# Kernel tuning notes

Measured on AMD Instinct MI355X. Metric: run time of the kernel, lower is better.

The kernel has to match this reference:

```python
import jax, jax.numpy as jnp
import numpy as np

N = 100000
E = 1600000
IN_DIM = 128
HID = 128
OUT_DIM = 128


def _glorot(key, shape):
    lim = jnp.sqrt(6.0 / (shape[0] + shape[1]))
    return jax.random.uniform(key, shape, jnp.float32, -lim, lim)


def setup_inputs() -> dict:
    key = jax.random.key(0)
    ks = jax.random.split(key, 8)
    x = jax.random.normal(ks[0], (N, IN_DIM), jnp.float32)
    edge_index = jax.random.randint(ks[1], (2, E), 0, N, jnp.int64)
    # layer 1 (SAGEConv(in_dim, hid)): lin_l applied to mean-aggregated neighbors (with bias),
    # lin_r applied to root features (no bias) -- PyG SAGEConv semantics.
    W1l = _glorot(ks[2], (IN_DIM, HID))
    b1l = jnp.zeros((HID,), jnp.float32)
    W1r = _glorot(ks[3], (IN_DIM, HID))
    # layer 2 (SAGEConv(hid, out_dim))
    W2l = _glorot(ks[4], (HID, OUT_DIM))
    b2l = jnp.zeros((OUT_DIM,), jnp.float32)
    W2r = _glorot(ks[5], (HID, OUT_DIM))
    return {"x": x, "edge_index": edge_index,
            "W1l": W1l, "b1l": b1l, "W1r": W1r,
            "W2l": W2l, "b2l": b2l, "W2r": W2r}


def _sage_conv(h, src, dst, Wl, bl, Wr):
    # mean aggregation of source features onto target nodes
    msg_sum = jax.ops.segment_sum(h[src], dst, num_segments=N)  # [N, d]
    deg = jax.ops.segment_sum(jnp.ones((src.shape[0],), h.dtype), dst, num_segments=N)
    agg = msg_sum / jnp.maximum(deg, 1.0)[:, None]
    return agg @ Wl + bl + h @ Wr


def reference(x, edge_index, W1l, b1l, W1r, W2l, b2l, W2r):
    src = edge_index[0]
    dst = edge_index[1]
    h = jax.nn.relu(_sage_conv(x, src, dst, W1l, b1l, W1r))
    h = _sage_conv(h, src, dst, W2l, b2l, W2r)
    return h
```

## Files before the change

### kernel.cpp

```cpp
#include <hip/hip_runtime.h>
#include <cstdint>
#include <cstddef>

#define NN 100000
#define EE 1600000
#define DIM 128
#define CAP 48
#define OVF_CAP 512

#define NB 391
#define BCAP 4608
#define SLOTS 32
#define FLUSH_AT 16
#define ACHUNK 4096

typedef __attribute__((ext_vector_type(8))) short bf16x8;
typedef __attribute__((ext_vector_type(4))) float f32x4;

__device__ __forceinline__ unsigned short f2bf(float f) {
  union { float f; uint32_t u; } v; v.f = f;
  uint32_t r = v.u + 0x7FFF + ((v.u >> 16) & 1);
  return (unsigned short)(r >> 16);
}
__device__ __forceinline__ float bf2f(unsigned short s) {
  union { uint32_t u; float f; } v; v.u = (uint32_t)s << 16;
  return v.f;
}
__device__ __forceinline__ float uaf(uint32_t u) {
  union { uint32_t u; float f; } v; v.u = u;
  return v.f;
}

__global__ __launch_bounds__(256) void partA_kernel(
    const void* __restrict__ edges, int* __restrict__ bcnt,
    unsigned* __restrict__ part, int* __restrict__ novf, int* __restrict__ ovf) {
  __shared__ unsigned stage[NB][SLOTS + 1];
  __shared__ int scnt[NB];
  __shared__ int sh_i64;
  const int t = threadIdx.x;
  for (int b = t; b < NB; b += 256) scnt[b] = 0;
  if (t < 64) {
    int v = ((const int*)edges)[2 * t + 1];
    unsigned long long m = __ballot(v != 0);
    if (t == 0) sh_i64 = (m == 0ull) ? 1 : 0;
  }
  __syncthreads();
  const int i64 = sh_i64;
  const long long ebase = (long long)blockIdx.x * ACHUNK;
  const int nrounds = ACHUNK / 256;
  for (int r = 0; r < nrounds; ++r) {
    long long e = ebase + (long long)r * 256 + t;
    if (e < EE) {
      int s, d;
      if (i64) {
        s = (int)((const long long*)edges)[e];
        d = (int)((const long long*)edges)[(long long)EE + e];
      } else {
        s = ((const int*)edges)[e];
        d = ((const int*)edges)[(long long)EE + e];
      }
      if ((unsigned)s < NN && (unsigned)d < NN) {
        int b = d >> 8;
        unsigned pk = (unsigned)s | ((unsigned)(d & 255) << 17);
        int pos = atomicAdd(&scnt[b], 1);
        if (pos < SLOTS) {
          stage[b][pos] = pk;
        } else {
          int g = atomicAdd(&bcnt[b], 1);
          if (g < BCAP) part[(size_t)b * BCAP + g] = pk;
          else { int oi = atomicAdd(novf, 1); if (oi < OVF_CAP) { ovf[oi*2] = s; ovf[oi*2+1] = d; } }
        }
      }
    }
    __syncthreads();
    const bool last = (r == nrounds - 1);
    for (int b = t; b < NB; b += 256) {
      int c = scnt[b];
      if (c > SLOTS) c = SLOTS;
      if (c > 0 && (last || c >= FLUSH_AT)) {
        int g = atomicAdd(&bcnt[b], c);
        for (int i = 0; i < c; ++i) {
          int gp = g + i;
          unsigned pk = stage[b][i];
          if (gp < BCAP) {
            part[(size_t)b * BCAP + gp] = pk;
          } else {
            int oi = atomicAdd(novf, 1);
            if (oi < OVF_CAP) { ovf[oi*2] = (int)(pk & 0x1FFFF); ovf[oi*2+1] = (b << 8) | (int)(pk >> 17); }
          }
        }
        scnt[b] = 0;
      }
    }
    __syncthreads();
  }
}

__global__ __launch_bounds__(256) void partB_kernel(
    const int* __restrict__ bcnt, const unsigned* __restrict__ part,
    int* __restrict__ cnt, int* __restrict__ ell,
    int* __restrict__ novf, int* __restrict__ ovf) {
  __shared__ int lcnt[256];
  __shared__ int lell[256 * CAP];
  const int t = threadIdx.x;
  const int b = blockIdx.x;
  lcnt[t] = 0;
  __syncthreads();
  int n = bcnt[b];
  if (n > BCAP) n = BCAP;
  for (int i = t; i < n; i += 256) {
    unsigned pk = part[(size_t)b * BCAP + i];
    int s = (int)(pk & 0x1FFFF);
    int dl = (int)(pk >> 17);
    int pos = atomicAdd(&lcnt[dl], 1);
    if (pos < CAP) lell[dl * CAP + pos] = s;
    else { int oi = atomicAdd(novf, 1); if (oi < OVF_CAP) { ovf[oi*2] = s; ovf[oi*2+1] = (b << 8) | dl; } }
  }
  __syncthreads();
  int4* dst = (int4*)(ell + (size_t)b * 256 * CAP);
  const int4* src = (const int4*)lell;
#pragma unroll
  for (int i = 0; i < 256 * CAP / 4 / 256; ++i) dst[t + i * 256] = src[t + i * 256];
  int node = b * 256 + t;
  if (node < NN) cnt[node] = lcnt[t];
}

__global__ void prep_kernel(const float* __restrict__ x,
                            const float* __restrict__ W1l, const float* __restrict__ W1r,
                            const float* __restrict__ W2l, const float* __restrict__ W2r,
                            unsigned short* __restrict__ Wt1, unsigned short* __restrict__ Wt2,
                            unsigned short* __restrict__ xhi) {
  if (blockIdx.x < 256) {
    int idx = blockIdx.x * 256 + threadIdx.x;
    int layer = idx >> 15;
    int rest = idx & 32767;
    int mat = rest >> 14;
    int r = rest & 16383;
    int k = r >> 7, n = r & 127;
    const float* W = layer ? (mat ? W2r : W2l) : (mat ? W1r : W1l);
    unsigned short* Wt = layer ? Wt2 : Wt1;
    Wt[((size_t)(mat * 128 + n)) * 128 + k] = f2bf(W[k * 128 + n]);
  } else {
    int i = (blockIdx.x - 256) * 256 + threadIdx.x;
    if (i >= NN * DIM / 4) return;
    f32x4 v = ((const f32x4*)x)[i];
    ushort4 hi;
    hi.x = f2bf(v[0]); hi.y = f2bf(v[1]); hi.z = f2bf(v[2]); hi.w = f2bf(v[3]);
    ((ushort4*)xhi)[i] = hi;
  }
}

__device__ __forceinline__ void acc_dw4(float* s, uint4 w) {
  s[0] += uaf(w.x << 16); s[1] += uaf(w.x & 0xFFFF0000u);
  s[2] += uaf(w.y << 16); s[3] += uaf(w.y & 0xFFFF0000u);
  s[4] += uaf(w.z << 16); s[5] += uaf(w.z & 0xFFFF0000u);
  s[6] += uaf(w.w << 16); s[7] += uaf(w.w & 0xFFFF0000u);
}

__global__ __launch_bounds__(256) void gather_ell_kernel(
    const int* __restrict__ cnt, const int* __restrict__ ell,
    const unsigned short* __restrict__ h, unsigned short* __restrict__ ahi,
    const int* __restrict__ novf, const int* __restrict__ ovf) {
  const int node = blockIdx.x * 4 + (threadIdx.x >> 6);
  const int lane = threadIdx.x & 63;
  const int q = lane >> 4;
  const int l = lane & 15;
  if (node >= NN) return;
  const int dcnt = cnt[node];
  const int n = dcnt < CAP ? dcnt : CAP;
  const int* row = ell + (size_t)node * CAP;
  float s[8] = {0.f, 0.f, 0.f, 0.f, 0.f, 0.f, 0.f, 0.f};
  int p = q;
  for (; p + 12 < n; p += 16) {
    uint4 w0 = *(const uint4*)(h + (size_t)row[p] * DIM + l * 8);
    uint4 w1 = *(const uint4*)(h + (size_t)row[p + 4] * DIM + l * 8);
    uint4 w2 = *(const uint4*)(h + (size_t)row[p + 8] * DIM + l * 8);
    uint4 w3 = *(const uint4*)(h + (size_t)row[p + 12] * DIM + l * 8);
    acc_dw4(s, w0);
    acc_dw4(s, w1);
    acc_dw4(s, w2);
    acc_dw4(s, w3);
  }
  for (; p < n; p += 4) {
    uint4 w0 = *(const uint4*)(h + (size_t)row[p] * DIM + l * 8);
    acc_dw4(s, w0);
  }
#pragma unroll
  for (int i = 0; i < 8; ++i) {
    s[i] += __shfl_xor(s[i], 16, 64);
    s[i] += __shfl_xor(s[i], 32, 64);
  }
  if (q == 0) {
    if (dcnt > CAP) {
      int no = *novf;
      if (no > OVF_CAP) no = OVF_CAP;
      for (int i = 0; i < no; ++i) {
        if (ovf[i * 2 + 1] == node) {
          uint4 w0 = *(const uint4*)(h + (size_t)ovf[i * 2] * DIM + l * 8);
          acc_dw4(s, w0);
        }
      }
    }
    const float rd = 1.0f / fmaxf((float)dcnt, 1.0f);
    ushort4 o0, o1;
    o0.x = f2bf(s[0] * rd); o0.y = f2bf(s[1] * rd);
    o0.z = f2bf(s[2] * rd); o0.w = f2bf(s[3] * rd);
    o1.x = f2bf(s[4] * rd); o1.y = f2bf(s[5] * rd);
    o1.z = f2bf(s[6] * rd); o1.w = f2bf(s[7] * rd);
    *(ushort4*)(ahi + (size_t)node * DIM + l * 8) = o0;
    *(ushort4*)(ahi + (size_t)node * DIM + l * 8 + 4) = o1;
  }
}

template <bool RELU, bool WPLANES, bool WOUT>
__global__ __launch_bounds__(256, 2) void dense_mfma_kernel(
    const unsigned short* __restrict__ ahi, const unsigned short* __restrict__ hhi,
    const unsigned short* __restrict__ Wt, const float* __restrict__ bl,
    float* __restrict__ out, unsigned short* __restrict__ phi, int n) {
  const int t = threadIdx.x;
  const int wave = t >> 6, lane = t & 63;
  const int l15 = lane & 15, l4 = lane >> 4;
  const int base = blockIdx.x * 64;

  bf16x8 bfr[2][4][2];
#pragma unroll
  for (int mat = 0; mat < 2; ++mat)
#pragma unroll
    for (int kt = 0; kt < 4; ++kt)
#pragma unroll
      for (int ntl = 0; ntl < 2; ++ntl) {
        int ncol = (wave * 2 + ntl) * 16 + l15;
        int k0 = kt * 32 + l4 * 8;
        bfr[mat][kt][ntl] = *(const bf16x8*)(Wt + ((size_t)(mat * 128 + ncol)) * 128 + k0);
      }

  f32x4 acc[4][2];
#pragma unroll
  for (int ntl = 0; ntl < 2; ++ntl) {
    float b = bl[(wave * 2 + ntl) * 16 + l15];
#pragma unroll
    for (int rt = 0; rt < 4; ++rt) {
      f32x4 ib = {b, b, b, b};
      acc[rt][ntl] = ib;
    }
  }

#pragma unroll
  for (int kt = 0; kt < 4; ++kt) {
    const int k0 = kt * 32 + l4 * 8;
#pragma unroll
    for (int rt = 0; rt < 4; ++rt) {
      int row = base + rt * 16 + l15;
      if (row >= n) row = n - 1;
      const size_t off = (size_t)row * DIM + k0;
      bf16x8 a8 = *(const bf16x8*)(ahi + off);
      bf16x8 hh8 = *(const bf16x8*)(hhi + off);
#pragma unroll
      for (int ntl = 0; ntl < 2; ++ntl) {
        acc[rt][ntl] = __builtin_amdgcn_mfma_f32_16x16x32_bf16(a8, bfr[0][kt][ntl], acc[rt][ntl], 0, 0, 0);
        acc[rt][ntl] = __builtin_amdgcn_mfma_f32_16x16x32_bf16(hh8, bfr[1][kt][ntl], acc[rt][ntl], 0, 0, 0);
      }
    }
  }

  __syncthreads();

#pragma unroll
  for (int rt = 0; rt < 4; ++rt)
#pragma unroll
    for (int ntl = 0; ntl < 2; ++ntl) {
      const int col = (wave * 2 + ntl) * 16 + l15;
#pragma unroll
      for (int r = 0; r < 4; ++r) {
        int row = base + rt * 16 + l4 * 4 + r;
        if (row < n) {
          float v = acc[rt][ntl][r];
          if (RELU) v = fmaxf(v, 0.f);
          const size_t off = (size_t)row * DIM + col;
          if (WOUT) out[off] = v;
          if (WPLANES) phi[off] = f2bf(v);
        }
      }
    }
}

extern "C" void kernel_launch(void* const* d_in, const int* in_sizes, int n_in,
                              void* d_out, int out_size, void* d_ws, size_t ws_size,
                              hipStream_t stream) {
  const float* x   = (const float*)d_in[0];
  const void* edges = d_in[1];
  const float* W1l = (const float*)d_in[2];
  const float* b1l = (const float*)d_in[3];
  const float* W1r = (const float*)d_in[4];
  const float* W2l = (const float*)d_in[5];
  const float* b2l = (const float*)d_in[6];
  const float* W2r = (const float*)d_in[7];
  float* out = (float*)d_out;

  char* p = (char*)d_ws;
  unsigned short* Wt1 = (unsigned short*)p;               p += 2 * 128 * 128 * 2;
  unsigned short* Wt2 = (unsigned short*)p;               p += 2 * 128 * 128 * 2;
  int* cnt  = (int*)p;                                    p += (size_t)NN * 4;
  int* bcnt = (int*)p;                                    p += (size_t)NB * 4;
  int* novf = (int*)p;                                    p += 4;
  p = (char*)(((uintptr_t)p + 15) & ~(uintptr_t)15);
  int* ovf = (int*)p;                                     p += (size_t)OVF_CAP * 2 * 4;
  p = (char*)(((uintptr_t)p + 255) & ~(uintptr_t)255);
  int* ell = (int*)p;                                     p += (size_t)NB * 256 * CAP * 4;
  p = (char*)(((uintptr_t)p + 255) & ~(uintptr_t)255);
  unsigned short* hhi = (unsigned short*)p;               p += (size_t)NN * DIM * 2;
  unsigned short* ahi = (unsigned short*)p;               p += (size_t)NN * DIM * 2;
  unsigned* part = (unsigned*)ahi;

  hipMemsetAsync(bcnt, 0, ((size_t)NB + 1) * 4, stream);

  partA_kernel<<<(EE + ACHUNK - 1) / ACHUNK, 256, 0, stream>>>(edges, bcnt, part, novf, ovf);
  partB_kernel<<<NB, 256, 0, stream>>>(bcnt, part, cnt, ell, novf, ovf);

  prep_kernel<<<256 + NN * DIM / 4 / 256, 256, 0, stream>>>(x, W1l, W1r, W2l, W2r, Wt1, Wt2, hhi);

  const int gather_blocks = (NN + 3) / 4;
  const int dense_blocks = (NN + 63) / 64;

  gather_ell_kernel<<<gather_blocks, 256, 0, stream>>>(cnt, ell, hhi, ahi, novf, ovf);
  dense_mfma_kernel<true, true, false><<<dense_blocks, 256, 0, stream>>>(
      ahi, hhi, Wt1, b1l, out, hhi, NN);

  gather_ell_kernel<<<gather_blocks, 256, 0, stream>>>(cnt, ell, hhi, ahi, novf, ovf);
  dense_mfma_kernel<false, false, true><<<dense_blocks, 256, 0, stream>>>(
      ahi, hhi, Wt2, b2l, out, nullptr, NN);
}
```

Measured before the change: 270.3 us.

## Fuse neighbor gather with MFMA dense layer and merge prep into partition kernel

The gather and the dense MFMA kernels are merged into one per-layer kernel. Each block aggregates 64 nodes (two nodes per wave iteration) into a swizzled LDS tile, then runs the bf16 MFMA GEMM reading A from LDS, which removes the global round-trip of the aggregated matrix. The weight/x bf16 prep work is folded into the edge partition kernel as extra blocks, and that kernel now runs 512 threads per block, which saves a launch. Layer-2 reads go to a separate hh1 buffer so they no longer alias hx. Risks are lower gather parallelism per block, load imbalance across nodes with different degrees, and weights being reloaded per k-tile instead of being held in registers.

```diff
diff --git a/kernel.cpp b/kernel.cpp
--- a/kernel.cpp
+++ b/kernel.cpp
@@ -13,6 +13,10 @@
 #define SLOTS 32
 #define FLUSH_AT 16
 #define ACHUNK 4096
+#define ATHREADS 512
+
+#define NPREP_W 128
+#define NPREP_X ((NN * DIM / 4) / ATHREADS)
 
 typedef __attribute__((ext_vector_type(8))) short bf16x8;
 typedef __attribute__((ext_vector_type(4))) float f32x4;
@@ -22,23 +26,58 @@
   uint32_t r = v.u + 0x7FFF + ((v.u >> 16) & 1);
   return (unsigned short)(r >> 16);
 }
-__device__ __forceinline__ float bf2f(unsigned short s) {
-  union { uint32_t u; float f; } v; v.u = (uint32_t)s << 16;
-  return v.f;
-}
 __device__ __forceinline__ float uaf(uint32_t u) {
   union { uint32_t u; float f; } v; v.u = u;
   return v.f;
 }
-
-__global__ __launch_bounds__(256) void partA_kernel(
+__device__ __forceinline__ uint32_t pk2(float a, float b) {
+  return (uint32_t)f2bf(a) | ((uint32_t)f2bf(b) << 16);
+}
+__device__ __forceinline__ void acc_dw4(float* s, uint4 w) {
+  s[0] += uaf(w.x << 16); s[1] += uaf(w.x & 0xFFFF0000u);
+  s[2] += uaf(w.y << 16); s[3] += uaf(w.y & 0xFFFF0000u);
+  s[4] += uaf(w.z << 16); s[5] += uaf(w.z & 0xFFFF0000u);
+  s[6] += uaf(w.w << 16); s[7] += uaf(w.w & 0xFFFF0000u);
+}
+
+__global__ __launch_bounds__(ATHREADS) void partA_prep_kernel(
     const void* __restrict__ edges, int* __restrict__ bcnt,
-    unsigned* __restrict__ part, int* __restrict__ novf, int* __restrict__ ovf) {
+    unsigned* __restrict__ part, int* __restrict__ novf, int* __restrict__ ovf,
+    const float* __restrict__ x,
+    const float* __restrict__ W1l, const float* __restrict__ W1r,
+    const float* __restrict__ W2l, const float* __restrict__ W2r,
+    unsigned short* __restrict__ Wt1, unsigned short* __restrict__ Wt2,
+    unsigned short* __restrict__ xhi) {
   __shared__ unsigned stage[NB][SLOTS + 1];
   __shared__ int scnt[NB];
   __shared__ int sh_i64;
   const int t = threadIdx.x;
-  for (int b = t; b < NB; b += 256) scnt[b] = 0;
+
+  if (blockIdx.x >= NB) {
+    int bid = blockIdx.x - NB;
+    if (bid < NPREP_W) {
+      int idx = bid * ATHREADS + t;
+      int layer = idx >> 15;
+      int rest = idx & 32767;
+      int mat = rest >> 14;
+      int r = rest & 16383;
+      int k = r >> 7, n = r & 127;
+      const float* W = layer ? (mat ? W2r : W2l) : (mat ? W1r : W1l);
+      unsigned short* Wt = layer ? Wt2 : Wt1;
+      Wt[((size_t)(mat * 128 + n)) * 128 + k] = f2bf(W[k * 128 + n]);
+    } else {
+      int i = (bid - NPREP_W) * ATHREADS + t;
+      if (i < NN * DIM / 4) {
+        f32x4 v = ((const f32x4*)x)[i];
+        ushort4 hi;
+        hi.x = f2bf(v[0]); hi.y = f2bf(v[1]); hi.z = f2bf(v[2]); hi.w = f2bf(v[3]);
+        ((ushort4*)xhi)[i] = hi;
+      }
+    }
+    return;
+  }
+
+  for (int b = t; b < NB; b += ATHREADS) scnt[b] = 0;
   if (t < 64) {
     int v = ((const int*)edges)[2 * t + 1];
     unsigned long long m = __ballot(v != 0);
@@ -47,9 +86,9 @@
   __syncthreads();
   const int i64 = sh_i64;
   const long long ebase = (long long)blockIdx.x * ACHUNK;
-  const int nrounds = ACHUNK / 256;
+  const int nrounds = ACHUNK / ATHREADS;
   for (int r = 0; r < nrounds; ++r) {
-    long long e = ebase + (long long)r * 256 + t;
+    long long e = ebase + (long long)r * ATHREADS + t;
     if (e < EE) {
       int s, d;
       if (i64) {
@@ -74,7 +113,7 @@
     }
     __syncthreads();
     const bool last = (r == nrounds - 1);
-    for (int b = t; b < NB; b += 256) {
+    for (int b = t; b < NB; b += ATHREADS) {
       int c = scnt[b];
       if (c > SLOTS) c = SLOTS;
       if (c > 0 && (last || c >= FLUSH_AT)) {
@@ -125,115 +164,85 @@
   if (node < NN) cnt[node] = lcnt[t];
 }
 
-__global__ void prep_kernel(const float* __restrict__ x,
-                            const float* __restrict__ W1l, const float* __restrict__ W1r,
-                            const float* __restrict__ W2l, const float* __restrict__ W2r,
-                            unsigned short* __restrict__ Wt1, unsigned short* __restrict__ Wt2,
-                            unsigned short* __restrict__ xhi) {
-  if (blockIdx.x < 256) {
-    int idx = blockIdx.x * 256 + threadIdx.x;
-    int layer = idx >> 15;
-    int rest = idx & 32767;
-    int mat = rest >> 14;
-    int r = rest & 16383;
-    int k = r >> 7, n = r & 127;
-    const float* W = layer ? (mat ? W2r : W2l) : (mat ? W1r : W1l);
-    unsigned short* Wt = layer ? Wt2 : Wt1;
-    Wt[((size_t)(mat * 128 + n)) * 128 + k] = f2bf(W[k * 128 + n]);
-  } else {
-    int i = (blockIdx.x - 256) * 256 + threadIdx.x;
-    if (i >= NN * DIM / 4) return;
-    f32x4 v = ((const f32x4*)x)[i];
-    ushort4 hi;
-    hi.x = f2bf(v[0]); hi.y = f2bf(v[1]); hi.z = f2bf(v[2]); hi.w = f2bf(v[3]);
-    ((ushort4*)xhi)[i] = hi;
-  }
-}
-
-__device__ __forceinline__ void acc_dw4(float* s, uint4 w) {
-  s[0] += uaf(w.x << 16); s[1] += uaf(w.x & 0xFFFF0000u);
-  s[2] += uaf(w.y << 16); s[3] += uaf(w.y & 0xFFFF0000u);
-  s[4] += uaf(w.z << 16); s[5] += uaf(w.z & 0xFFFF0000u);
-  s[6] += uaf(w.w << 16); s[7] += uaf(w.w & 0xFFFF0000u);
-}
-
-__global__ __launch_bounds__(256) void gather_ell_kernel(
+template <bool RELU, bool WPLANES, bool WOUT>
+__global__ __launch_bounds__(256, 3) void fused_kernel(
     const int* __restrict__ cnt, const int* __restrict__ ell,
-    const unsigned short* __restrict__ h, unsigned short* __restrict__ ahi,
+    const unsigned short* __restrict__ h, const unsigned short* __restrict__ Wt,
+    const float* __restrict__ bl, float* __restrict__ out,
+    unsigned short* __restrict__ ph,
     const int* __restrict__ novf, const int* __restrict__ ovf) {
-  const int node = blockIdx.x * 4 + (threadIdx.x >> 6);
-  const int lane = threadIdx.x & 63;
+  __shared__ unsigned short lds_a[64 * DIM];
+  const int t = threadIdx.x;
+  const int wave = t >> 6, lane = t & 63;
   const int q = lane >> 4;
   const int l = lane & 15;
-  if (node >= NN) return;
-  const int dcnt = cnt[node];
-  const int n = dcnt < CAP ? dcnt : CAP;
-  const int* row = ell + (size_t)node * CAP;
-  float s[8] = {0.f, 0.f, 0.f, 0.f, 0.f, 0.f, 0.f, 0.f};
-  int p = q;
-  for (; p + 12 < n; p += 16) {
-    uint4 w0 = *(const uint4*)(h + (size_t)row[p] * DIM + l * 8);
-    uint4 w1 = *(const uint4*)(h + (size_t)row[p + 4] * DIM + l * 8);
-    uint4 w2 = *(const uint4*)(h + (size_t)row[p + 8] * DIM + l * 8);
-    uint4 w3 = *(const uint4*)(h + (size_t)row[p + 12] * DIM + l * 8);
-    acc_dw4(s, w0);
-    acc_dw4(s, w1);
-    acc_dw4(s, w2);
-    acc_dw4(s, w3);
-  }
-  for (; p < n; p += 4) {
-    uint4 w0 = *(const uint4*)(h + (size_t)row[p] * DIM + l * 8);
-    acc_dw4(s, w0);
-  }
-#pragma unroll
-  for (int i = 0; i < 8; ++i) {
-    s[i] += __shfl_xor(s[i], 16, 64);
-    s[i] += __shfl_xor(s[i], 32, 64);
-  }
-  if (q == 0) {
-    if (dcnt > CAP) {
-      int no = *novf;
-      if (no > OVF_CAP) no = OVF_CAP;
-      for (int i = 0; i < no; ++i) {
-        if (ovf[i * 2 + 1] == node) {
-          uint4 w0 = *(const uint4*)(h + (size_t)ovf[i * 2] * DIM + l * 8);
-          acc_dw4(s, w0);
+  const int base = blockIdx.x * 64;
+
+  for (int i = 0; i < 16; i += 2) {
+    const int nl0 = wave * 16 + i;
+    const int nl1 = nl0 + 1;
+    const int node0 = base + nl0, node1 = base + nl1;
+    const int dc0 = (node0 < NN) ? cnt[node0] : 0;
+    const int dc1 = (node1 < NN) ? cnt[node1] : 0;
+    const int n0 = dc0 < CAP ? dc0 : CAP;
+    const int n1 = dc1 < CAP ? dc1 : CAP;
+    const int* r0 = ell + (size_t)node0 * CAP;
+    const int* r1 = ell + (size_t)node1 * CAP;
+    float s0[8] = {0.f,0.f,0.f,0.f,0.f,0.f,0.f,0.f};
+    float s1[8] = {0.f,0.f,0.f,0.f,0.f,0.f,0.f,0.f};
+    const int nmax = n0 > n1 ? n0 : n1;
+    for (int p = q; p < nmax; p += 16) {
+      uint4 w[8];
+#pragma unroll
+      for (int j = 0; j < 4; ++j)
+        if (p + j * 4 < n0) w[j] = *(const uint4*)(h + (size_t)r0[p + j * 4] * DIM + l * 8);
+#pragma unroll
+      for (int j = 0; j < 4; ++j)
+        if (p + j * 4 < n1) w[4 + j] = *(const uint4*)(h + (size_t)r1[p + j * 4] * DIM + l * 8);
+#pragma unroll
+      for (int j = 0; j < 4; ++j)
+        if (p + j * 4 < n0) acc_dw4(s0, w[j]);
+#pragma unroll
+      for (int j = 0; j < 4; ++j)
+        if (p + j * 4 < n1) acc_dw4(s1, w[4 + j]);
+    }
+#pragma unroll
+    for (int k = 0; k < 8; ++k) {
+      s0[k] += __shfl_xor(s0[k], 16, 64);
+      s0[k] += __shfl_xor(s0[k], 32, 64);
+      s1[k] += __shfl_xor(s1[k], 16, 64);
+      s1[k] += __shfl_xor(s1[k], 32, 64);
+    }
+    if (q == 0) {
+      if (dc0 > CAP || dc1 > CAP) {
+        int no = *novf;
+        if (no > OVF_CAP) no = OVF_CAP;
+        for (int k = 0; k < no; ++k) {
+          int od = ovf[k * 2 + 1];
+          if (od == node0 && dc0 > CAP) {
+            uint4 w = *(const uint4*)(h + (size_t)ovf[k * 2] * DIM + l * 8);
+            acc_dw4(s0, w);
+          }
+          if (od == node1 && dc1 > CAP) {
+            uint4 w = *(const uint4*)(h + (size_t)ovf[k * 2] * DIM + l * 8);
+            acc_dw4(s1, w);
+          }
         }
       }
-    }
-    const float rd = 1.0f / fmaxf((float)dcnt, 1.0f);
-    ushort4 o0, o1;
-    o0.x = f2bf(s[0] * rd); o0.y = f2bf(s[1] * rd);
-    o0.z = f2bf(s[2] * rd); o0.w = f2bf(s[3] * rd);
-    o1.x = f2bf(s[4] * rd); o1.y = f2bf(s[5] * rd);
-    o1.z = f2bf(s[6] * rd); o1.w = f2bf(s[7] * rd);
-    *(ushort4*)(ahi + (size_t)node * DIM + l * 8) = o0;
-    *(ushort4*)(ahi + (size_t)node * DIM + l * 8 + 4) = o1;
-  }
-}
-
-template <bool RELU, bool WPLANES, bool WOUT>
-__global__ __launch_bounds__(256, 2) void dense_mfma_kernel(
-    const unsigned short* __restrict__ ahi, const unsigned short* __restrict__ hhi,
-    const unsigned short* __restrict__ Wt, const float* __restrict__ bl,
-    float* __restrict__ out, unsigned short* __restrict__ phi, int n) {
-  const int t = threadIdx.x;
-  const int wave = t >> 6, lane = t & 63;
+      const float rd0 = 1.0f / fmaxf((float)dc0, 1.0f);
+      const float rd1 = 1.0f / fmaxf((float)dc1, 1.0f);
+      uint4 pk0, pk1;
+      pk0.x = pk2(s0[0]*rd0, s0[1]*rd0); pk0.y = pk2(s0[2]*rd0, s0[3]*rd0);
+      pk0.z = pk2(s0[4]*rd0, s0[5]*rd0); pk0.w = pk2(s0[6]*rd0, s0[7]*rd0);
+      pk1.x = pk2(s1[0]*rd1, s1[1]*rd1); pk1.y = pk2(s1[2]*rd1, s1[3]*rd1);
+      pk1.z = pk2(s1[4]*rd1, s1[5]*rd1); pk1.w = pk2(s1[6]*rd1, s1[7]*rd1);
+      *(uint4*)(lds_a + nl0 * DIM + (l ^ (nl0 & 15)) * 8) = pk0;
+      *(uint4*)(lds_a + nl1 * DIM + (l ^ (nl1 & 15)) * 8) = pk1;
+    }
+  }
+  __syncthreads();
+
   const int l15 = lane & 15, l4 = lane >> 4;
-  const int base = blockIdx.x * 64;
-
-  bf16x8 bfr[2][4][2];
-#pragma unroll
-  for (int mat = 0; mat < 2; ++mat)
-#pragma unroll
-    for (int kt = 0; kt < 4; ++kt)
-#pragma unroll
-      for (int ntl = 0; ntl < 2; ++ntl) {
-        int ncol = (wave * 2 + ntl) * 16 + l15;
-        int k0 = kt * 32 + l4 * 8;
-        bfr[mat][kt][ntl] = *(const bf16x8*)(Wt + ((size_t)(mat * 128 + ncol)) * 128 + k0);
-      }
-
   f32x4 acc[4][2];
 #pragma unroll
   for (int ntl = 0; ntl < 2; ++ntl) {
@@ -248,22 +257,28 @@
 #pragma unroll
   for (int kt = 0; kt < 4; ++kt) {
     const int k0 = kt * 32 + l4 * 8;
+    bf16x8 b0[2], b1[2];
+#pragma unroll
+    for (int ntl = 0; ntl < 2; ++ntl) {
+      int ncol = (wave * 2 + ntl) * 16 + l15;
+      b0[ntl] = *(const bf16x8*)(Wt + (size_t)ncol * 128 + k0);
+      b1[ntl] = *(const bf16x8*)(Wt + (size_t)(128 + ncol) * 128 + k0);
+    }
 #pragma unroll
     for (int rt = 0; rt < 4; ++rt) {
-      int row = base + rt * 16 + l15;
-      if (row >= n) row = n - 1;
-      const size_t off = (size_t)row * DIM + k0;
-      bf16x8 a8 = *(const bf16x8*)(ahi + off);
-      bf16x8 hh8 = *(const bf16x8*)(hhi + off);
+      const int r = rt * 16 + l15;
+      const int chunk = (kt * 4 + l4) ^ l15;
+      bf16x8 a8 = *(const bf16x8*)(lds_a + r * DIM + chunk * 8);
+      int row = base + r;
+      if (row >= NN) row = NN - 1;
+      bf16x8 hh8 = *(const bf16x8*)(h + (size_t)row * DIM + k0);
 #pragma unroll
       for (int ntl = 0; ntl < 2; ++ntl) {
-        acc[rt][ntl] = __builtin_amdgcn_mfma_f32_16x16x32_bf16(a8, bfr[0][kt][ntl], acc[rt][ntl], 0, 0, 0);
-        acc[rt][ntl] = __builtin_amdgcn_mfma_f32_16x16x32_bf16(hh8, bfr[1][kt][ntl], acc[rt][ntl], 0, 0, 0);
-      }
-    }
-  }
-
-  __syncthreads();
+        acc[rt][ntl] = __builtin_amdgcn_mfma_f32_16x16x32_bf16(a8, b0[ntl], acc[rt][ntl], 0, 0, 0);
+        acc[rt][ntl] = __builtin_amdgcn_mfma_f32_16x16x32_bf16(hh8, b1[ntl], acc[rt][ntl], 0, 0, 0);
+      }
+    }
+  }
 
 #pragma unroll
   for (int rt = 0; rt < 4; ++rt)
@@ -273,12 +288,12 @@
 #pragma unroll
       for (int r = 0; r < 4; ++r) {
         int row = base + rt * 16 + l4 * 4 + r;
-        if (row < n) {
+        if (row < NN) {
           float v = acc[rt][ntl][r];
           if (RELU) v = fmaxf(v, 0.f);
           const size_t off = (size_t)row * DIM + col;
           if (WOUT) out[off] = v;
-          if (WPLANES) phi[off] = f2bf(v);
+          if (WPLANES) ph[off] = f2bf(v);
         }
       }
     }
@@ -308,25 +323,21 @@
   p = (char*)(((uintptr_t)p + 255) & ~(uintptr_t)255);
   int* ell = (int*)p;                                     p += (size_t)NB * 256 * CAP * 4;
   p = (char*)(((uintptr_t)p + 255) & ~(uintptr_t)255);
-  unsigned short* hhi = (unsigned short*)p;               p += (size_t)NN * DIM * 2;
-  unsigned short* ahi = (unsigned short*)p;               p += (size_t)NN * DIM * 2;
-  unsigned* part = (unsigned*)ahi;
+  unsigned short* hx  = (unsigned short*)p;               p += (size_t)NN * DIM * 2;
+  unsigned short* hh1 = (unsigned short*)p;               p += (size_t)NN * DIM * 2;
+  unsigned* part = (unsigned*)hh1;
 
   hipMemsetAsync(bcnt, 0, ((size_t)NB + 1) * 4, stream);
 
-  partA_kernel<<<(EE + ACHUNK - 1) / ACHUNK, 256, 0, stream>>>(edges, bcnt, part, novf, ovf);
+  partA_prep_kernel<<<NB + NPREP_W + NPREP_X, ATHREADS, 0, stream>>>(
+      edges, bcnt, part, novf, ovf, x, W1l, W1r, W2l, W2r, Wt1, Wt2, hx);
   partB_kernel<<<NB, 256, 0, stream>>>(bcnt, part, cnt, ell, novf, ovf);
 
-  prep_kernel<<<256 + NN * DIM / 4 / 256, 256, 0, stream>>>(x, W1l, W1r, W2l, W2r, Wt1, Wt2, hhi);
-
-  const int gather_blocks = (NN + 3) / 4;
-  const int dense_blocks = (NN + 63) / 64;
-
-  gather_ell_kernel<<<gather_blocks, 256, 0, stream>>>(cnt, ell, hhi, ahi, novf, ovf);
-  dense_mfma_kernel<true, true, false><<<dense_blocks, 256, 0, stream>>>(
-      ahi, hhi, Wt1, b1l, out, hhi, NN);
-
-  gather_ell_kernel<<<gather_blocks, 256, 0, stream>>>(cnt, ell, hhi, ahi, novf, ovf);
-  dense_mfma_kernel<false, false, true><<<dense_blocks, 256, 0, stream>>>(
-      ahi, hhi, Wt2, b2l, out, nullptr, NN);
-}
+  const int fused_blocks = (NN + 63) / 64;
+
+  fused_kernel<true, true, false><<<fused_blocks, 256, 0, stream>>>(
+      cnt, ell, hx, Wt1, b1l, out, hh1, novf, ovf);
+
+  fused_kernel<false, false, true><<<fused_blocks, 256, 0, stream>>>(
+      cnt, ell, hh1, Wt2, b2l, out, nullptr, novf, ovf);
+}
```

After: 267.9 us (median of 2 runs). Within noise of the previous version (-0.9%).
